# Kernel optimization log

Hardware: AMD Instinct MI355X
Metric: run time of the kernel (lower is better)

The kernel has to match this reference:

```python
import jax, jax.numpy as jnp
import numpy as np

EMBED_DIM = 64
HIDDEN_DIM = 320
CONTEXT_DIM = 768

def setup_inputs() -> dict:
    key = jax.random.key(0)
    k1, k2, k3, k4, k5 = jax.random.split(key, 5)
    B, T, S = 4, 4096, 4096
    tokens = jax.random.normal(k1, (B, T, HIDDEN_DIM), dtype=jnp.float32)
    context = jax.random.normal(k2, (B, S, CONTEXT_DIM), dtype=jnp.float32)
    # nn.Linear(in, out, bias=False) weights, stored as [out, in] like torch
    sq = 1.0 / np.sqrt(HIDDEN_DIM)
    sk = 1.0 / np.sqrt(CONTEXT_DIM)
    Wq = jax.random.uniform(k3, (EMBED_DIM, HIDDEN_DIM), minval=-sq, maxval=sq, dtype=jnp.float32)
    Wk = jax.random.uniform(k4, (EMBED_DIM, CONTEXT_DIM), minval=-sk, maxval=sk, dtype=jnp.float32)
    Wv = jax.random.uniform(k5, (HIDDEN_DIM, CONTEXT_DIM), minval=-sk, maxval=sk, dtype=jnp.float32)
    return {"tokens": tokens, "context": context, "Wq": Wq, "Wk": Wk, "Wv": Wv}

def reference(tokens, context, Wq, Wk, Wv):
    # Q: [B,T,E], K: [B,S,E], V: [B,S,Hd]
    Q = jnp.einsum('bth,eh->bte', tokens, Wq)
    K = jnp.einsum('bsc,ec->bse', context, Wk)
    V = jnp.einsum('bsc,hc->bsh', context, Wv)
    scores = jnp.einsum('bte,bse->bts', Q, K) / np.sqrt(EMBED_DIM)
    attn = jax.nn.softmax(scores, axis=-1)  # [B,T,S] full score matrix as in original
    ctx_vecs = jnp.einsum('bts,bsh->bth', attn, V)
    return ctx_vecs
```

## Files before the change

kernel.cpp:

```cpp
#include <hip/hip_runtime.h>
#include <hip/hip_bf16.h>

typedef _Float16 half4_t  __attribute__((ext_vector_type(4)));
typedef _Float16 half8_t  __attribute__((ext_vector_type(8)));
typedef float    float4_t __attribute__((ext_vector_type(4)));

#define MFMA16x32(a, b, c) __builtin_amdgcn_mfma_f32_16x16x32_f16(a, b, c, 0, 0, 0)

static constexpr int Tn = 4096, Sn = 4096, Hn = 320;

__device__ __forceinline__ void async16(const _Float16* g, _Float16* l) {
  __builtin_amdgcn_global_load_lds(
      (const __attribute__((address_space(1))) void*)g,
      (__attribute__((address_space(3))) void*)l, 16, 0, 0);
}

template <int KTOT, int NT>
__global__ __launch_bounds__(256, 2)
void proj_kernel(const float* __restrict__ A, const float* __restrict__ W,
                 _Float16* __restrict__ out, float sc) {
  constexpr int NCH = KTOT / 64;
  constexpr int NTIL = NT / 16;
  __shared__ alignas(16) _Float16 Ach[64 * 72];
  __shared__ alignas(16) _Float16 Bch[NT * 72];

  const int tid = threadIdx.x, w = tid >> 6, lane = tid & 63;
  const int G = lane >> 4, l15 = lane & 15;
  const int m0 = blockIdx.x * 64, n0 = blockIdx.y * NT;

  float4_t acc[NTIL];
#pragma unroll
  for (int nt = 0; nt < NTIL; ++nt) acc[nt] = {0.f, 0.f, 0.f, 0.f};

  float4_t areg[4], wreg[NTIL];
  auto ldA = [&](int kc) {
#pragma unroll
    for (int t = 0; t < 4; ++t) {
      int idx = t * 256 + tid;
      areg[t] = *(const float4_t*)(A + (size_t)(m0 + (idx >> 4)) * KTOT + kc * 64 + (idx & 15) * 4);
    }
  };
  auto ldW = [&](int kc) {
#pragma unroll
    for (int t = 0; t < NTIL; ++t) {
      int idx = t * 256 + tid;
      wreg[t] = *(const float4_t*)(W + (size_t)(n0 + (idx >> 4)) * KTOT + kc * 64 + (idx & 15) * 4);
    }
  };

  ldA(0); ldW(0);
  for (int kc = 0; kc < NCH; ++kc) {
    __syncthreads();
#pragma unroll
    for (int t = 0; t < 4; ++t) {
      int idx = t * 256 + tid;
      half4_t h = {(_Float16)areg[t][0], (_Float16)areg[t][1], (_Float16)areg[t][2], (_Float16)areg[t][3]};
      *(half4_t*)(Ach + (idx >> 4) * 72 + (idx & 15) * 4) = h;
    }
#pragma unroll
    for (int t = 0; t < NTIL; ++t) {
      int idx = t * 256 + tid;
      half4_t h = {(_Float16)wreg[t][0], (_Float16)wreg[t][1], (_Float16)wreg[t][2], (_Float16)wreg[t][3]};
      *(half4_t*)(Bch + (idx >> 4) * 72 + (idx & 15) * 4) = h;
    }
    __syncthreads();
    if (kc + 1 < NCH) { ldA(kc + 1); ldW(kc + 1); }
#pragma unroll
    for (int c = 0; c < 2; ++c) {
      half8_t af = *(const half8_t*)(Ach + (w * 16 + l15) * 72 + c * 32 + 8 * G);
#pragma unroll
      for (int nt = 0; nt < NTIL; ++nt) {
        half8_t bf = *(const half8_t*)(Bch + (nt * 16 + l15) * 72 + c * 32 + 8 * G);
        acc[nt] = MFMA16x32(af, bf, acc[nt]);
      }
    }
  }

  if constexpr (NT == 64) {
#pragma unroll
    for (int nt = 0; nt < NTIL; ++nt)
#pragma unroll
      for (int r = 0; r < 4; ++r)
        out[(size_t)(m0 + w * 16 + 4 * G + r) * 64 + nt * 16 + l15] = (_Float16)(acc[nt][r] * sc);
  } else {
    __syncthreads();
#pragma unroll
    for (int nt = 0; nt < NTIL; ++nt) {
      half4_t h = {(_Float16)acc[nt][0], (_Float16)acc[nt][1], (_Float16)acc[nt][2], (_Float16)acc[nt][3]};
      *(half4_t*)(Bch + (nt * 16 + l15) * 72 + w * 16 + 4 * G) = h;
    }
    __syncthreads();
#pragma unroll
    for (int rep = 0; rep < 5; ++rep) {
      int idx = w * 5 + rep;
      int c2 = idx / 10, htl = idx % 10;
      half8_t fr = *(const half8_t*)(Bch + (htl * 16 + l15) * 72 + c2 * 32 + 8 * G);
      int sg = m0 + c2 * 32;
      int b = sg >> 12, c2b = (sg & 4095) >> 5;
      int htg = blockIdx.y * 10 + htl;
      *(half8_t*)(out + ((size_t)((b * 128 + c2b) * 20 + htg)) * 512 + lane * 8) = fr;
    }
  }
}

__global__ __launch_bounds__(256, 2)
void flash_kernel(const _Float16* __restrict__ Qg, const _Float16* __restrict__ Kg,
                  const _Float16* __restrict__ Vt, _Float16* __restrict__ Op,
                  float* __restrict__ lp) {
  __shared__ alignas(16) _Float16 kbuf[32 * 72];
  __shared__ alignas(16) _Float16 pbuf[64 * 72];
  __shared__ alignas(16) _Float16 vbuf[2][10240];
  __shared__ float lred[4][32];

  const int tid = threadIdx.x, w = tid >> 6, lane = tid & 63;
  const int G = lane >> 4, l15 = lane & 15;
  const int bx = blockIdx.x;
  const int b = (bx & 7) >> 1, sh = bx & 1, tb = bx >> 3;
  const int tblk = tb * 64, sbase = sh * 2048;
  const int th = w >> 1, stile = w & 1;
  const int kr = tid >> 3, kc8 = (tid & 7) * 8;

  half8_t qf[2][2];
#pragma unroll
  for (int tt = 0; tt < 2; ++tt)
#pragma unroll
    for (int c = 0; c < 2; ++c)
      qf[tt][c] = *(const half8_t*)(Qg + (size_t)(b * Tn + tblk + th * 32 + tt * 16 + l15) * 64 + c * 32 + 8 * G);

  float4_t oacc[2][5][2];
  float4_t oa[4][5];
#pragma unroll
  for (int tt = 0; tt < 4; ++tt)
#pragma unroll
    for (int ht = 0; ht < 5; ++ht) oa[tt][ht] = {0.f, 0.f, 0.f, 0.f};
  float la[2] = {0.f, 0.f};

  const size_t vbase = (size_t)b * 1310720;

  {
    uint4 k0 = *(const uint4*)(Kg + (size_t)(b * Sn + sbase + kr) * 64 + kc8);
    *(uint4*)(&kbuf[kr * 72 + kc8]) = k0;
    const size_t voff = vbase + (size_t)(sh * 64) * 10240;
#pragma unroll
    for (int r = 0; r < 5; ++r) {
      int off = (w * 5 + r) * 512 + lane * 8;
      async16(Vt + voff + off, &vbuf[0][off]);
    }
  }
  __syncthreads();

  for (int n = 0; n < 64; ++n) {
    const int cb = n & 1;
    const bool more = (n < 63);
    uint4 kst;
    if (more)
      kst = *(const uint4*)(Kg + (size_t)(b * Sn + sbase + (n + 1) * 32 + kr) * 64 + kc8);

    float4_t sa[2] = {{0.f, 0.f, 0.f, 0.f}, {0.f, 0.f, 0.f, 0.f}};
#pragma unroll
    for (int c = 0; c < 2; ++c) {
      half8_t af = *(const half8_t*)(&kbuf[(stile * 16 + l15) * 72 + c * 32 + 8 * G]);
#pragma unroll
      for (int tt = 0; tt < 2; ++tt) sa[tt] = MFMA16x32(af, qf[tt][c], sa[tt]);
    }
#pragma unroll
    for (int tt = 0; tt < 2; ++tt) {
      float e0 = exp2f(sa[tt][0]), e1 = exp2f(sa[tt][1]);
      float e2 = exp2f(sa[tt][2]), e3 = exp2f(sa[tt][3]);
      la[tt] += (e0 + e1) + (e2 + e3);
      half4_t p = {(_Float16)e0, (_Float16)e1, (_Float16)e2, (_Float16)e3};
      *(half4_t*)(&pbuf[(th * 32 + tt * 16 + l15) * 72 + stile * 16 + 4 * G]) = p;
    }
    __syncthreads();

    if (more) {
      const size_t voff = vbase + (size_t)(sh * 64 + n + 1) * 10240;
#pragma unroll
      for (int r = 0; r < 5; ++r) {
        int off = (w * 5 + r) * 512 + lane * 8;
        async16(Vt + voff + off, &vbuf[1 - cb][off]);
      }
      *(uint4*)(&kbuf[kr * 72 + kc8]) = kst;
    }

    half8_t pa[4];
#pragma unroll
    for (int tt = 0; tt < 4; ++tt)
      pa[tt] = *(const half8_t*)(&pbuf[(tt * 16 + l15) * 72 + 8 * G]);
#pragma unroll
    for (int ht = 0; ht < 5; ++ht) {
      half8_t vb = *(const half8_t*)(&vbuf[cb][(w * 5 + ht) * 512 + lane * 8]);
#pragma unroll
      for (int tt = 0; tt < 4; ++tt) oa[tt][ht] = MFMA16x32(pa[tt], vb, oa[tt][ht]);
    }
    __syncthreads();
  }

#pragma unroll
  for (int tt = 0; tt < 2; ++tt) {
    float v = la[tt];
    v += __shfl_xor(v, 16);
    v += __shfl_xor(v, 32);
    if (lane < 16) lred[w][tt * 16 + lane] = v;
  }
  __syncthreads();
  if (stile == 0 && lane < 16) {
#pragma unroll
    for (int tt = 0; tt < 2; ++tt) {
      float lt = lred[w][tt * 16 + lane] + lred[w + 1][tt * 16 + lane];
      lp[(size_t)sh * 16384 + b * Tn + tblk + th * 32 + tt * 16 + lane] = lt;
    }
  }
  _Float16* myO = Op + (size_t)sh * 5242880;
#pragma unroll
  for (int tt = 0; tt < 4; ++tt)
#pragma unroll
    for (int ht = 0; ht < 5; ++ht)
#pragma unroll
      for (int r = 0; r < 4; ++r)
        myO[(size_t)(b * Tn + tblk + tt * 16 + 4 * G + r) * Hn + w * 80 + ht * 16 + l15] =
            (_Float16)oa[tt][ht][r];
}

__global__ __launch_bounds__(256)
void combine_kernel(const _Float16* __restrict__ O0, const _Float16* __restrict__ O1,
                    const float* __restrict__ l0, const float* __restrict__ l1,
                    float* __restrict__ out) {
  const int tid = threadIdx.x;
  const int base = blockIdx.x * 1280;
#pragma unroll
  for (int it = 0; it < 5; ++it) {
    int lin = base + it * 256 + tid;
    int row = lin / 80;
    float inv = 1.0f / (l0[row] + l1[row]);
    half4_t a = *(const half4_t*)(O0 + (size_t)lin * 4);
    half4_t c = *(const half4_t*)(O1 + (size_t)lin * 4);
    float4_t o = {((float)a[0] + (float)c[0]) * inv, ((float)a[1] + (float)c[1]) * inv,
                  ((float)a[2] + (float)c[2]) * inv, ((float)a[3] + (float)c[3]) * inv};
    *(float4_t*)(out + (size_t)lin * 4) = o;
  }
}

extern "C" void kernel_launch(void* const* d_in, const int* in_sizes, int n_in,
                              void* d_out, int out_size, void* d_ws, size_t ws_size,
                              hipStream_t stream) {
  const float* tokens  = (const float*)d_in[0];
  const float* context = (const float*)d_in[1];
  const float* Wq      = (const float*)d_in[2];
  const float* Wk      = (const float*)d_in[3];
  const float* Wv      = (const float*)d_in[4];

  _Float16* Qws = (_Float16*)d_ws;
  _Float16* Kws = Qws + (size_t)1048576;
  _Float16* Vws = Kws + (size_t)1048576;
  _Float16* O0  = Vws + (size_t)5242880;
  _Float16* O1  = O0 + (size_t)5242880;
  float*    l0  = (float*)(O1 + (size_t)5242880);
  float*    l1  = l0 + 16384;

  const float qsc = 0.125f * 1.44269504088896f;
  proj_kernel<320, 64><<<dim3(256, 1), 256, 0, stream>>>(tokens, Wq, Qws, qsc);
  proj_kernel<768, 64><<<dim3(256, 1), 256, 0, stream>>>(context, Wk, Kws, 1.0f);
  proj_kernel<768, 160><<<dim3(256, 2), 256, 0, stream>>>(context, Wv, Vws, 1.0f);
  flash_kernel<<<dim3(512), 256, 0, stream>>>(Qws, Kws, Vws, O0, l0);
  combine_kernel<<<dim3(1024), 256, 0, stream>>>(O0, O1, l0, l1, (float*)d_out);
}
```

Measured before the change: 229.6 us.

## Fuse QKV projections, warp-specialize flash kernel, drop split-S combine

The three projection launches become one kernel that dispatches on block index. The flash kernel now uses 512-thread blocks where four warps compute QK^T and exp while four warps do PV with register-prefetched V, ping-ponged through double-buffered LDS. Each block walks the full S range, so the split-S partial outputs and the separate combine kernel go away, and normalization happens in the epilogue with fp32 output. This cuts launches and intermediate traffic but halves the grid to 256 blocks and doubles the serial loop length per block.

```diff
diff --git a/kernel.cpp b/kernel.cpp
--- a/kernel.cpp
+++ b/kernel.cpp
@@ -7,26 +7,16 @@
 
 #define MFMA16x32(a, b, c) __builtin_amdgcn_mfma_f32_16x16x32_f16(a, b, c, 0, 0, 0)
 
-static constexpr int Tn = 4096, Sn = 4096, Hn = 320;
-
-__device__ __forceinline__ void async16(const _Float16* g, _Float16* l) {
-  __builtin_amdgcn_global_load_lds(
-      (const __attribute__((address_space(1))) void*)g,
-      (__attribute__((address_space(3))) void*)l, 16, 0, 0);
-}
-
-template <int KTOT, int NT>
-__global__ __launch_bounds__(256, 2)
-void proj_kernel(const float* __restrict__ A, const float* __restrict__ W,
-                 _Float16* __restrict__ out, float sc) {
+template <int KTOT, int NT, int MODE>
+__device__ __forceinline__ void proj_body(const float* __restrict__ A,
+                                          const float* __restrict__ W,
+                                          _Float16* __restrict__ out, float sc,
+                                          int m0, int n0, int htg0,
+                                          _Float16* Ach, _Float16* Bch) {
   constexpr int NCH = KTOT / 64;
   constexpr int NTIL = NT / 16;
-  __shared__ alignas(16) _Float16 Ach[64 * 72];
-  __shared__ alignas(16) _Float16 Bch[NT * 72];
-
   const int tid = threadIdx.x, w = tid >> 6, lane = tid & 63;
   const int G = lane >> 4, l15 = lane & 15;
-  const int m0 = blockIdx.x * 64, n0 = blockIdx.y * NT;
 
   float4_t acc[NTIL];
 #pragma unroll
@@ -76,7 +66,7 @@
     }
   }
 
-  if constexpr (NT == 64) {
+  if constexpr (MODE <= 1) {
 #pragma unroll
     for (int nt = 0; nt < NTIL; ++nt)
 #pragma unroll
@@ -97,147 +87,167 @@
       half8_t fr = *(const half8_t*)(Bch + (htl * 16 + l15) * 72 + c2 * 32 + 8 * G);
       int sg = m0 + c2 * 32;
       int b = sg >> 12, c2b = (sg & 4095) >> 5;
-      int htg = blockIdx.y * 10 + htl;
+      int htg = htg0 + htl;
       *(half8_t*)(out + ((size_t)((b * 128 + c2b) * 20 + htg)) * 512 + lane * 8) = fr;
     }
   }
 }
 
 __global__ __launch_bounds__(256, 2)
+void qkv_proj_kernel(const float* __restrict__ tokens, const float* __restrict__ context,
+                     const float* __restrict__ Wq, const float* __restrict__ Wk,
+                     const float* __restrict__ Wv, _Float16* __restrict__ Q,
+                     _Float16* __restrict__ K, _Float16* __restrict__ V) {
+  __shared__ alignas(16) _Float16 smem[16128];
+  _Float16* Ach = smem;
+  _Float16* Bch = smem + 64 * 72;
+  const int bx = blockIdx.x;
+  const float qsc = 0.125f * 1.44269504088896f;
+  if (bx < 512) {
+    int y = bx >> 8, mb = bx & 255;
+    proj_body<768, 160, 2>(context, Wv, V, 1.0f, mb * 64, y * 160, y * 10, Ach, Bch);
+  } else if (bx < 768) {
+    proj_body<768, 64, 1>(context, Wk, K, 1.0f, (bx - 512) * 64, 0, 0, Ach, Bch);
+  } else {
+    proj_body<320, 64, 0>(tokens, Wq, Q, qsc, (bx - 768) * 64, 0, 0, Ach, Bch);
+  }
+}
+
+__global__ __launch_bounds__(512, 2)
 void flash_kernel(const _Float16* __restrict__ Qg, const _Float16* __restrict__ Kg,
-                  const _Float16* __restrict__ Vt, _Float16* __restrict__ Op,
-                  float* __restrict__ lp) {
-  __shared__ alignas(16) _Float16 kbuf[32 * 72];
-  __shared__ alignas(16) _Float16 pbuf[64 * 72];
-  __shared__ alignas(16) _Float16 vbuf[2][10240];
-  __shared__ float lred[4][32];
+                  const _Float16* __restrict__ Vt, float* __restrict__ out) {
+  __shared__ alignas(16) _Float16 kbuf[2][2048];
+  __shared__ alignas(16) _Float16 pbuf[2][2048];
+  __shared__ float larr[2][4][16];
+  __shared__ float linv[64];
 
   const int tid = threadIdx.x, w = tid >> 6, lane = tid & 63;
   const int G = lane >> 4, l15 = lane & 15;
   const int bx = blockIdx.x;
-  const int b = (bx & 7) >> 1, sh = bx & 1, tb = bx >> 3;
-  const int tblk = tb * 64, sbase = sh * 2048;
-  const int th = w >> 1, stile = w & 1;
-  const int kr = tid >> 3, kc8 = (tid & 7) * 8;
+  const int b = (bx & 7) >> 1;
+  const int tblk = ((bx & 1) * 32 + (bx >> 3)) * 64;
+
+  const bool is_pv = (w < 4);
+  const int sw = w - 4;
+  const int stile = sw & 1, tthalf = sw >> 1;
+  const int t2 = tid & 255;
+  const int s_loc = t2 >> 3, e8 = t2 & 7;
+  const int kdst = ((s_loc >> 4) * 2 + (e8 >> 2)) * 512 + ((e8 & 3) * 16 + (s_loc & 15)) * 8;
+  const _Float16* kg = Kg + (size_t)(b * 4096) * 64 + s_loc * 64 + e8 * 8;
+  const _Float16* vt_b = Vt + (size_t)b * 1310720;
 
   half8_t qf[2][2];
-#pragma unroll
-  for (int tt = 0; tt < 2; ++tt)
+  float la[2] = {0.f, 0.f};
+  float4_t oa[4][5];
+#pragma unroll
+  for (int tt = 0; tt < 4; ++tt)
+#pragma unroll
+    for (int ht = 0; ht < 5; ++ht) oa[tt][ht] = {0.f, 0.f, 0.f, 0.f};
+  half8_t vcur[5], vnxt[5];
+
+  if (!is_pv) {
+    uint4 k0 = *(const uint4*)(kg);
+    uint4 k1 = *(const uint4*)(kg + 2048);
+    *(uint4*)(&kbuf[0][kdst]) = k0;
+    *(uint4*)(&kbuf[1][kdst]) = k1;
+#pragma unroll
+    for (int tt2 = 0; tt2 < 2; ++tt2) {
+      int tt = tthalf * 2 + tt2;
+#pragma unroll
+      for (int c = 0; c < 2; ++c)
+        qf[tt2][c] = *(const half8_t*)(Qg + (size_t)(b * 4096 + tblk + tt * 16 + l15) * 64 + c * 32 + 8 * G);
+    }
+  }
+  __syncthreads();
+
+  if (is_pv) {
+#pragma unroll
+    for (int ht = 0; ht < 5; ++ht)
+      vcur[ht] = *(const half8_t*)(vt_b + (w * 5 + ht) * 512 + lane * 8);
+  } else {
+    half8_t af[2];
 #pragma unroll
     for (int c = 0; c < 2; ++c)
-      qf[tt][c] = *(const half8_t*)(Qg + (size_t)(b * Tn + tblk + th * 32 + tt * 16 + l15) * 64 + c * 32 + 8 * G);
-
-  float4_t oacc[2][5][2];
-  float4_t oa[4][5];
-#pragma unroll
-  for (int tt = 0; tt < 4; ++tt)
-#pragma unroll
-    for (int ht = 0; ht < 5; ++ht) oa[tt][ht] = {0.f, 0.f, 0.f, 0.f};
-  float la[2] = {0.f, 0.f};
-
-  const size_t vbase = (size_t)b * 1310720;
-
-  {
-    uint4 k0 = *(const uint4*)(Kg + (size_t)(b * Sn + sbase + kr) * 64 + kc8);
-    *(uint4*)(&kbuf[kr * 72 + kc8]) = k0;
-    const size_t voff = vbase + (size_t)(sh * 64) * 10240;
-#pragma unroll
-    for (int r = 0; r < 5; ++r) {
-      int off = (w * 5 + r) * 512 + lane * 8;
-      async16(Vt + voff + off, &vbuf[0][off]);
-    }
-  }
-  __syncthreads();
-
-  for (int n = 0; n < 64; ++n) {
-    const int cb = n & 1;
-    const bool more = (n < 63);
-    uint4 kst;
-    if (more)
-      kst = *(const uint4*)(Kg + (size_t)(b * Sn + sbase + (n + 1) * 32 + kr) * 64 + kc8);
-
-    float4_t sa[2] = {{0.f, 0.f, 0.f, 0.f}, {0.f, 0.f, 0.f, 0.f}};
-#pragma unroll
-    for (int c = 0; c < 2; ++c) {
-      half8_t af = *(const half8_t*)(&kbuf[(stile * 16 + l15) * 72 + c * 32 + 8 * G]);
-#pragma unroll
-      for (int tt = 0; tt < 2; ++tt) sa[tt] = MFMA16x32(af, qf[tt][c], sa[tt]);
-    }
-#pragma unroll
-    for (int tt = 0; tt < 2; ++tt) {
-      float e0 = exp2f(sa[tt][0]), e1 = exp2f(sa[tt][1]);
-      float e2 = exp2f(sa[tt][2]), e3 = exp2f(sa[tt][3]);
-      la[tt] += (e0 + e1) + (e2 + e3);
+      af[c] = *(const half8_t*)(&kbuf[0][(stile * 2 + c) * 512 + lane * 8]);
+#pragma unroll
+    for (int tt2 = 0; tt2 < 2; ++tt2) {
+      float4_t sa = {0.f, 0.f, 0.f, 0.f};
+#pragma unroll
+      for (int c = 0; c < 2; ++c) sa = MFMA16x32(af[c], qf[tt2][c], sa);
+      float e0 = exp2f(sa[0]), e1 = exp2f(sa[1]), e2 = exp2f(sa[2]), e3 = exp2f(sa[3]);
+      la[tt2] += (e0 + e1) + (e2 + e3);
+      int tt = tthalf * 2 + tt2;
+      int Gp = stile * 2 + (G >> 1);
       half4_t p = {(_Float16)e0, (_Float16)e1, (_Float16)e2, (_Float16)e3};
-      *(half4_t*)(&pbuf[(th * 32 + tt * 16 + l15) * 72 + stile * 16 + 4 * G]) = p;
-    }
-    __syncthreads();
-
-    if (more) {
-      const size_t voff = vbase + (size_t)(sh * 64 + n + 1) * 10240;
-#pragma unroll
-      for (int r = 0; r < 5; ++r) {
-        int off = (w * 5 + r) * 512 + lane * 8;
-        async16(Vt + voff + off, &vbuf[1 - cb][off]);
-      }
-      *(uint4*)(&kbuf[kr * 72 + kc8]) = kst;
-    }
-
-    half8_t pa[4];
+      *(half4_t*)(&pbuf[0][tt * 512 + (Gp * 16 + l15) * 8 + 4 * (G & 1)]) = p;
+    }
+  }
+  __syncthreads();
+
+  for (int i = 0; i < 128; ++i) {
+    if (is_pv) {
+      if (i < 127) {
+#pragma unroll
+        for (int ht = 0; ht < 5; ++ht)
+          vnxt[ht] = *(const half8_t*)(vt_b + (size_t)(i + 1) * 10240 + (w * 5 + ht) * 512 + lane * 8);
+      }
+      half8_t pa[4];
+#pragma unroll
+      for (int tt = 0; tt < 4; ++tt)
+        pa[tt] = *(const half8_t*)(&pbuf[i & 1][tt * 512 + lane * 8]);
+#pragma unroll
+      for (int ht = 0; ht < 5; ++ht)
+#pragma unroll
+        for (int tt = 0; tt < 4; ++tt) oa[tt][ht] = MFMA16x32(pa[tt], vcur[ht], oa[tt][ht]);
+#pragma unroll
+      for (int ht = 0; ht < 5; ++ht) vcur[ht] = vnxt[ht];
+    } else if (i < 127) {
+      uint4 kreg;
+      if (i < 126) kreg = *(const uint4*)(kg + (size_t)(i + 2) * 2048);
+      half8_t af[2];
+#pragma unroll
+      for (int c = 0; c < 2; ++c)
+        af[c] = *(const half8_t*)(&kbuf[(i + 1) & 1][(stile * 2 + c) * 512 + lane * 8]);
+#pragma unroll
+      for (int tt2 = 0; tt2 < 2; ++tt2) {
+        float4_t sa = {0.f, 0.f, 0.f, 0.f};
+#pragma unroll
+        for (int c = 0; c < 2; ++c) sa = MFMA16x32(af[c], qf[tt2][c], sa);
+        float e0 = exp2f(sa[0]), e1 = exp2f(sa[1]), e2 = exp2f(sa[2]), e3 = exp2f(sa[3]);
+        la[tt2] += (e0 + e1) + (e2 + e3);
+        int tt = tthalf * 2 + tt2;
+        int Gp = stile * 2 + (G >> 1);
+        half4_t p = {(_Float16)e0, (_Float16)e1, (_Float16)e2, (_Float16)e3};
+        *(half4_t*)(&pbuf[(i + 1) & 1][tt * 512 + (Gp * 16 + l15) * 8 + 4 * (G & 1)]) = p;
+      }
+      if (i < 126) *(uint4*)(&kbuf[i & 1][kdst]) = kreg;
+    }
+    __syncthreads();
+  }
+
+  if (!is_pv) {
+#pragma unroll
+    for (int tt2 = 0; tt2 < 2; ++tt2) {
+      float v = la[tt2];
+      v += __shfl_xor(v, 16);
+      v += __shfl_xor(v, 32);
+      if (lane < 16) larr[stile][tthalf * 2 + tt2][l15] = v;
+    }
+  }
+  __syncthreads();
+  if (tid < 64) linv[tid] = 1.0f / (larr[0][tid >> 4][tid & 15] + larr[1][tid >> 4][tid & 15]);
+  __syncthreads();
+  if (is_pv) {
 #pragma unroll
     for (int tt = 0; tt < 4; ++tt)
-      pa[tt] = *(const half8_t*)(&pbuf[(tt * 16 + l15) * 72 + 8 * G]);
-#pragma unroll
-    for (int ht = 0; ht < 5; ++ht) {
-      half8_t vb = *(const half8_t*)(&vbuf[cb][(w * 5 + ht) * 512 + lane * 8]);
-#pragma unroll
-      for (int tt = 0; tt < 4; ++tt) oa[tt][ht] = MFMA16x32(pa[tt], vb, oa[tt][ht]);
-    }
-    __syncthreads();
-  }
-
-#pragma unroll
-  for (int tt = 0; tt < 2; ++tt) {
-    float v = la[tt];
-    v += __shfl_xor(v, 16);
-    v += __shfl_xor(v, 32);
-    if (lane < 16) lred[w][tt * 16 + lane] = v;
-  }
-  __syncthreads();
-  if (stile == 0 && lane < 16) {
-#pragma unroll
-    for (int tt = 0; tt < 2; ++tt) {
-      float lt = lred[w][tt * 16 + lane] + lred[w + 1][tt * 16 + lane];
-      lp[(size_t)sh * 16384 + b * Tn + tblk + th * 32 + tt * 16 + lane] = lt;
-    }
-  }
-  _Float16* myO = Op + (size_t)sh * 5242880;
-#pragma unroll
-  for (int tt = 0; tt < 4; ++tt)
-#pragma unroll
-    for (int ht = 0; ht < 5; ++ht)
-#pragma unroll
-      for (int r = 0; r < 4; ++r)
-        myO[(size_t)(b * Tn + tblk + tt * 16 + 4 * G + r) * Hn + w * 80 + ht * 16 + l15] =
-            (_Float16)oa[tt][ht][r];
-}
-
-__global__ __launch_bounds__(256)
-void combine_kernel(const _Float16* __restrict__ O0, const _Float16* __restrict__ O1,
-                    const float* __restrict__ l0, const float* __restrict__ l1,
-                    float* __restrict__ out) {
-  const int tid = threadIdx.x;
-  const int base = blockIdx.x * 1280;
-#pragma unroll
-  for (int it = 0; it < 5; ++it) {
-    int lin = base + it * 256 + tid;
-    int row = lin / 80;
-    float inv = 1.0f / (l0[row] + l1[row]);
-    half4_t a = *(const half4_t*)(O0 + (size_t)lin * 4);
-    half4_t c = *(const half4_t*)(O1 + (size_t)lin * 4);
-    float4_t o = {((float)a[0] + (float)c[0]) * inv, ((float)a[1] + (float)c[1]) * inv,
-                  ((float)a[2] + (float)c[2]) * inv, ((float)a[3] + (float)c[3]) * inv};
-    *(float4_t*)(out + (size_t)lin * 4) = o;
+#pragma unroll
+      for (int r = 0; r < 4; ++r) {
+        float inv = linv[tt * 16 + 4 * G + r];
+        size_t row = (size_t)(b * 4096 + tblk + tt * 16 + 4 * G + r) * 320;
+#pragma unroll
+        for (int ht = 0; ht < 5; ++ht)
+          out[row + w * 80 + ht * 16 + l15] = oa[tt][ht][r] * inv;
+      }
   }
 }
 
@@ -253,15 +263,8 @@
   _Float16* Qws = (_Float16*)d_ws;
   _Float16* Kws = Qws + (size_t)1048576;
   _Float16* Vws = Kws + (size_t)1048576;
-  _Float16* O0  = Vws + (size_t)5242880;
-  _Float16* O1  = O0 + (size_t)5242880;
-  float*    l0  = (float*)(O1 + (size_t)5242880);
-  float*    l1  = l0 + 16384;
-
-  const float qsc = 0.125f * 1.44269504088896f;
-  proj_kernel<320, 64><<<dim3(256, 1), 256, 0, stream>>>(tokens, Wq, Qws, qsc);
-  proj_kernel<768, 64><<<dim3(256, 1), 256, 0, stream>>>(context, Wk, Kws, 1.0f);
-  proj_kernel<768, 160><<<dim3(256, 2), 256, 0, stream>>>(context, Wv, Vws, 1.0f);
-  flash_kernel<<<dim3(512), 256, 0, stream>>>(Qws, Kws, Vws, O0, l0);
-  combine_kernel<<<dim3(1024), 256, 0, stream>>>(O0, O1, l0, l1, (float*)d_out);
-}
+
+  qkv_proj_kernel<<<dim3(1024), 256, 0, stream>>>(tokens, context, Wq, Wk, Wv,
+                                                  Qws, Kws, Vws);
+  flash_kernel<<<dim3(256), 512, 0, stream>>>(Qws, Kws, Vws, (float*)d_out);
+}
```

Result: faster. 205.0 us (-10.7%).

## Fuse Q/K/V projections into one kernel and deepen flash pipeline with register V

Applied to the files above, without the earlier changes.

Adds a small kernel that casts the weights to fp16 once. The three projection launches are merged into one 512-thread kernel in which K and V share a single pass over the context rows, so context is read once instead of twice. The flash kernel now loads V straight into registers from the pre-tiled layout instead of async LDS copies, keeps a 4-deep K/P ring buffer in LDS with swizzled P indexing, and has one barrier per step instead of two. The price is higher register pressure and more complex prefetch logic, with clamped prefetch indices that issue some redundant loads at the tail.

```diff
diff --git a/kernel.cpp b/kernel.cpp
--- a/kernel.cpp
+++ b/kernel.cpp
@@ -7,99 +7,176 @@
 
 #define MFMA16x32(a, b, c) __builtin_amdgcn_mfma_f32_16x16x32_f16(a, b, c, 0, 0, 0)
 
-static constexpr int Tn = 4096, Sn = 4096, Hn = 320;
-
-__device__ __forceinline__ void async16(const _Float16* g, _Float16* l) {
-  __builtin_amdgcn_global_load_lds(
-      (const __attribute__((address_space(1))) void*)g,
-      (__attribute__((address_space(3))) void*)l, 16, 0, 0);
-}
-
-template <int KTOT, int NT>
-__global__ __launch_bounds__(256, 2)
-void proj_kernel(const float* __restrict__ A, const float* __restrict__ W,
-                 _Float16* __restrict__ out, float sc) {
-  constexpr int NCH = KTOT / 64;
-  constexpr int NTIL = NT / 16;
-  __shared__ alignas(16) _Float16 Ach[64 * 72];
-  __shared__ alignas(16) _Float16 Bch[NT * 72];
-
-  const int tid = threadIdx.x, w = tid >> 6, lane = tid & 63;
+__global__ __launch_bounds__(256)
+void wcast_kernel(const float* __restrict__ Wq, const float* __restrict__ Wk,
+                  const float* __restrict__ Wv, _Float16* __restrict__ Wqh,
+                  _Float16* __restrict__ Wkh, _Float16* __restrict__ Wvh) {
+  const int bx = blockIdx.x, tid = threadIdx.x;
+  const float* src; _Float16* dst; int idx;
+  if (bx < 20)       { src = Wq; dst = Wqh; idx = bx * 256 + tid; }
+  else if (bx < 68)  { src = Wk; dst = Wkh; idx = (bx - 20) * 256 + tid; }
+  else               { src = Wv; dst = Wvh; idx = (bx - 68) * 256 + tid; }
+  float4_t v = *(const float4_t*)(src + (size_t)idx * 4);
+  half4_t h = {(_Float16)v[0], (_Float16)v[1], (_Float16)v[2], (_Float16)v[3]};
+  *(half4_t*)(dst + (size_t)idx * 4) = h;
+}
+
+__global__ __launch_bounds__(512, 2)
+void proj_kernel(const float* __restrict__ tokens, const float* __restrict__ context,
+                 const _Float16* __restrict__ Wqh, const _Float16* __restrict__ Wkh,
+                 const _Float16* __restrict__ Wvh, _Float16* __restrict__ Qws,
+                 _Float16* __restrict__ Kws, _Float16* __restrict__ Vws) {
+  __shared__ alignas(16) _Float16 smem[20480];
+  _Float16* Ach = smem;
+  _Float16* Wch = smem + 5120;
+
+  const int bx = blockIdx.x, tid = threadIdx.x;
+  const int w = tid >> 6, lane = tid & 63;
   const int G = lane >> 4, l15 = lane & 15;
-  const int m0 = blockIdx.x * 64, n0 = blockIdx.y * NT;
-
-  float4_t acc[NTIL];
-#pragma unroll
-  for (int nt = 0; nt < NTIL; ++nt) acc[nt] = {0.f, 0.f, 0.f, 0.f};
-
-  float4_t areg[4], wreg[NTIL];
-  auto ldA = [&](int kc) {
-#pragma unroll
-    for (int t = 0; t < 4; ++t) {
-      int idx = t * 256 + tid;
-      areg[t] = *(const float4_t*)(A + (size_t)(m0 + (idx >> 4)) * KTOT + kc * 64 + (idx & 15) * 4);
-    }
-  };
-  auto ldW = [&](int kc) {
-#pragma unroll
-    for (int t = 0; t < NTIL; ++t) {
-      int idx = t * 256 + tid;
-      wreg[t] = *(const float4_t*)(W + (size_t)(n0 + (idx >> 4)) * KTOT + kc * 64 + (idx & 15) * 4);
-    }
-  };
-
-  ldA(0); ldW(0);
-  for (int kc = 0; kc < NCH; ++kc) {
+
+  if (bx < 128) {
+    const int m0 = bx * 128;
+    const int mg = w >> 2, ng = w & 3;
+
+    float4_t acc[4][6];
+#pragma unroll
+    for (int mi = 0; mi < 4; ++mi)
+#pragma unroll
+      for (int nt = 0; nt < 6; ++nt) acc[mi][nt] = {0.f, 0.f, 0.f, 0.f};
+
+    float4_t areg[2];
+    half8_t wreg[3];
+    auto ldA = [&](int kc) {
+#pragma unroll
+      for (int t = 0; t < 2; ++t) {
+        int slot = t * 512 + tid, row = slot >> 3, c4 = slot & 7;
+        areg[t] = *(const float4_t*)(context + (size_t)(m0 + row) * 768 + kc * 32 + c4 * 4);
+      }
+    };
+    auto ldW = [&](int kc) {
+#pragma unroll
+      for (int t = 0; t < 3; ++t) {
+        int slot = t * 512 + tid, row = slot >> 2, c8 = slot & 3;
+        const _Float16* p = (row < 64) ? (Wkh + (size_t)row * 768)
+                                       : (Wvh + (size_t)(row - 64) * 768);
+        wreg[t] = *(const half8_t*)(p + kc * 32 + c8 * 8);
+      }
+    };
+
+    ldA(0); ldW(0);
+    for (int kc = 0; kc < 24; ++kc) {
+      __syncthreads();
+#pragma unroll
+      for (int t = 0; t < 2; ++t) {
+        int slot = t * 512 + tid, row = slot >> 3, c4 = slot & 7;
+        half4_t h = {(_Float16)areg[t][0], (_Float16)areg[t][1],
+                     (_Float16)areg[t][2], (_Float16)areg[t][3]};
+        *(half4_t*)(Ach + row * 40 + c4 * 4) = h;
+      }
+#pragma unroll
+      for (int t = 0; t < 3; ++t) {
+        int slot = t * 512 + tid, row = slot >> 2, c8 = slot & 3;
+        *(half8_t*)(Wch + row * 40 + c8 * 8) = wreg[t];
+      }
+      __syncthreads();
+      if (kc + 1 < 24) { ldA(kc + 1); ldW(kc + 1); }
+      half8_t af[4], bf[6];
+#pragma unroll
+      for (int mi = 0; mi < 4; ++mi)
+        af[mi] = *(const half8_t*)(Ach + (mg * 64 + mi * 16 + l15) * 40 + 8 * G);
+#pragma unroll
+      for (int nt = 0; nt < 6; ++nt)
+        bf[nt] = *(const half8_t*)(Wch + ((ng * 6 + nt) * 16 + l15) * 40 + 8 * G);
+#pragma unroll
+      for (int mi = 0; mi < 4; ++mi)
+#pragma unroll
+        for (int nt = 0; nt < 6; ++nt) acc[mi][nt] = MFMA16x32(af[mi], bf[nt], acc[mi][nt]);
+    }
+
+    if (ng == 0) {
+#pragma unroll
+      for (int mi = 0; mi < 4; ++mi)
+#pragma unroll
+        for (int nt = 0; nt < 4; ++nt)
+#pragma unroll
+          for (int r = 0; r < 4; ++r)
+            Kws[(size_t)(m0 + mg * 64 + mi * 16 + 4 * G + r) * 64 + nt * 16 + l15] =
+                (_Float16)acc[mi][nt][r];
+    }
     __syncthreads();
-#pragma unroll
-    for (int t = 0; t < 4; ++t) {
-      int idx = t * 256 + tid;
-      half4_t h = {(_Float16)areg[t][0], (_Float16)areg[t][1], (_Float16)areg[t][2], (_Float16)areg[t][3]};
-      *(half4_t*)(Ach + (idx >> 4) * 72 + (idx & 15) * 4) = h;
-    }
-#pragma unroll
-    for (int t = 0; t < NTIL; ++t) {
-      int idx = t * 256 + tid;
-      half4_t h = {(_Float16)wreg[t][0], (_Float16)wreg[t][1], (_Float16)wreg[t][2], (_Float16)wreg[t][3]};
-      *(half4_t*)(Bch + (idx >> 4) * 72 + (idx & 15) * 4) = h;
-    }
-    __syncthreads();
-    if (kc + 1 < NCH) { ldA(kc + 1); ldW(kc + 1); }
-#pragma unroll
-    for (int c = 0; c < 2; ++c) {
-      half8_t af = *(const half8_t*)(Ach + (w * 16 + l15) * 72 + c * 32 + 8 * G);
-#pragma unroll
-      for (int nt = 0; nt < NTIL; ++nt) {
-        half8_t bf = *(const half8_t*)(Bch + (nt * 16 + l15) * 72 + c * 32 + 8 * G);
+    _Float16* scr = smem + w * 1152;
+    const int b = bx >> 5;
+#pragma unroll
+    for (int nt = 0; nt < 6; ++nt) {
+      int jt = ng * 6 + nt;
+      if (jt < 4) continue;
+      int htg = jt - 4;
+#pragma unroll
+      for (int mi = 0; mi < 4; ++mi) {
+        half4_t h = {(_Float16)acc[mi][nt][0], (_Float16)acc[mi][nt][1],
+                     (_Float16)acc[mi][nt][2], (_Float16)acc[mi][nt][3]};
+        *(half4_t*)(scr + l15 * 72 + mi * 16 + 4 * G) = h;
+      }
+#pragma unroll
+      for (int c2 = 0; c2 < 2; ++c2) {
+        half8_t fr = *(const half8_t*)(scr + l15 * 72 + c2 * 32 + 8 * G);
+        int c2b = (bx & 31) * 4 + mg * 2 + c2;
+        *(half8_t*)(Vws + ((size_t)((b * 128 + c2b) * 20 + htg)) * 512 + lane * 8) = fr;
+      }
+    }
+  } else {
+    const int m0 = (bx - 128) * 128;
+    const float qsc = 0.125f * 1.44269504088896f;
+
+    float4_t acc[4];
+#pragma unroll
+    for (int nt = 0; nt < 4; ++nt) acc[nt] = {0.f, 0.f, 0.f, 0.f};
+
+    float4_t areg[2];
+    half8_t wreg;
+    auto ldA = [&](int kc) {
+#pragma unroll
+      for (int t = 0; t < 2; ++t) {
+        int slot = t * 512 + tid, row = slot >> 3, c4 = slot & 7;
+        areg[t] = *(const float4_t*)(tokens + (size_t)(m0 + row) * 320 + kc * 32 + c4 * 4);
+      }
+    };
+    auto ldW = [&](int kc) {
+      if (tid < 256) {
+        int row = tid >> 2, c8 = tid & 3;
+        wreg = *(const half8_t*)(Wqh + (size_t)row * 320 + kc * 32 + c8 * 8);
+      }
+    };
+
+    ldA(0); ldW(0);
+    for (int kc = 0; kc < 10; ++kc) {
+      __syncthreads();
+#pragma unroll
+      for (int t = 0; t < 2; ++t) {
+        int slot = t * 512 + tid, row = slot >> 3, c4 = slot & 7;
+        half4_t h = {(_Float16)areg[t][0], (_Float16)areg[t][1],
+                     (_Float16)areg[t][2], (_Float16)areg[t][3]};
+        *(half4_t*)(Ach + row * 40 + c4 * 4) = h;
+      }
+      if (tid < 256) {
+        int row = tid >> 2, c8 = tid & 3;
+        *(half8_t*)(Wch + row * 40 + c8 * 8) = wreg;
+      }
+      __syncthreads();
+      if (kc + 1 < 10) { ldA(kc + 1); ldW(kc + 1); }
+      half8_t af = *(const half8_t*)(Ach + (w * 16 + l15) * 40 + 8 * G);
+#pragma unroll
+      for (int nt = 0; nt < 4; ++nt) {
+        half8_t bf = *(const half8_t*)(Wch + (nt * 16 + l15) * 40 + 8 * G);
         acc[nt] = MFMA16x32(af, bf, acc[nt]);
       }
     }
-  }
-
-  if constexpr (NT == 64) {
-#pragma unroll
-    for (int nt = 0; nt < NTIL; ++nt)
+#pragma unroll
+    for (int nt = 0; nt < 4; ++nt)
 #pragma unroll
       for (int r = 0; r < 4; ++r)
-        out[(size_t)(m0 + w * 16 + 4 * G + r) * 64 + nt * 16 + l15] = (_Float16)(acc[nt][r] * sc);
-  } else {
-    __syncthreads();
-#pragma unroll
-    for (int nt = 0; nt < NTIL; ++nt) {
-      half4_t h = {(_Float16)acc[nt][0], (_Float16)acc[nt][1], (_Float16)acc[nt][2], (_Float16)acc[nt][3]};
-      *(half4_t*)(Bch + (nt * 16 + l15) * 72 + w * 16 + 4 * G) = h;
-    }
-    __syncthreads();
-#pragma unroll
-    for (int rep = 0; rep < 5; ++rep) {
-      int idx = w * 5 + rep;
-      int c2 = idx / 10, htl = idx % 10;
-      half8_t fr = *(const half8_t*)(Bch + (htl * 16 + l15) * 72 + c2 * 32 + 8 * G);
-      int sg = m0 + c2 * 32;
-      int b = sg >> 12, c2b = (sg & 4095) >> 5;
-      int htg = blockIdx.y * 10 + htl;
-      *(half8_t*)(out + ((size_t)((b * 128 + c2b) * 20 + htg)) * 512 + lane * 8) = fr;
-    }
+        Qws[(size_t)(m0 + w * 16 + 4 * G + r) * 64 + nt * 16 + l15] =
+            (_Float16)(acc[nt][r] * qsc);
   }
 }
 
@@ -107,27 +184,34 @@
 void flash_kernel(const _Float16* __restrict__ Qg, const _Float16* __restrict__ Kg,
                   const _Float16* __restrict__ Vt, _Float16* __restrict__ Op,
                   float* __restrict__ lp) {
-  __shared__ alignas(16) _Float16 kbuf[32 * 72];
-  __shared__ alignas(16) _Float16 pbuf[64 * 72];
-  __shared__ alignas(16) _Float16 vbuf[2][10240];
-  __shared__ float lred[4][32];
+  __shared__ alignas(16) _Float16 kbuf[4 * 2048];
+  __shared__ alignas(16) _Float16 pbuf[4 * 2048];
+  __shared__ float larr[2][4][16];
 
   const int tid = threadIdx.x, w = tid >> 6, lane = tid & 63;
   const int G = lane >> 4, l15 = lane & 15;
   const int bx = blockIdx.x;
-  const int b = (bx & 7) >> 1, sh = bx & 1, tb = bx >> 3;
-  const int tblk = tb * 64, sbase = sh * 2048;
-  const int th = w >> 1, stile = w & 1;
-  const int kr = tid >> 3, kc8 = (tid & 7) * 8;
+  const int xcd = bx & 7, b = xcd >> 1, sh = xcd & 1;
+  const int tblk = (bx >> 3) * 64;
+  const int st = w & 1, th = w >> 1;
+
+  const int sB = tid >> 6, sL = tid & 63;
+  const int s_loc = (sB >> 1) * 16 + (sL & 15);
+  const int e0 = (sB & 1) * 32 + (sL >> 4) * 8;
+  const _Float16* kg = Kg + (size_t)(b * 4096 + sh * 2048 + s_loc) * 64 + e0;
+
+  const int pidx = (lane ^ ((lane >> 3) & 3)) * 8;
+  int idxp = (st * 2 + (G >> 1)) * 16 + l15;
+  idxp ^= (idxp >> 3) & 3;
+  const int pw = idxp * 8 + 4 * (G & 1);
 
   half8_t qf[2][2];
 #pragma unroll
-  for (int tt = 0; tt < 2; ++tt)
+  for (int tt2 = 0; tt2 < 2; ++tt2)
 #pragma unroll
     for (int c = 0; c < 2; ++c)
-      qf[tt][c] = *(const half8_t*)(Qg + (size_t)(b * Tn + tblk + th * 32 + tt * 16 + l15) * 64 + c * 32 + 8 * G);
-
-  float4_t oacc[2][5][2];
+      qf[tt2][c] = *(const half8_t*)(Qg + (size_t)(b * 4096 + tblk + (th * 2 + tt2) * 16 + l15) * 64 + c * 32 + 8 * G);
+
   float4_t oa[4][5];
 #pragma unroll
   for (int tt = 0; tt < 4; ++tt)
@@ -135,82 +219,84 @@
     for (int ht = 0; ht < 5; ++ht) oa[tt][ht] = {0.f, 0.f, 0.f, 0.f};
   float la[2] = {0.f, 0.f};
 
-  const size_t vbase = (size_t)b * 1310720;
-
-  {
-    uint4 k0 = *(const uint4*)(Kg + (size_t)(b * Sn + sbase + kr) * 64 + kc8);
-    *(uint4*)(&kbuf[kr * 72 + kc8]) = k0;
-    const size_t voff = vbase + (size_t)(sh * 64) * 10240;
-#pragma unroll
-    for (int r = 0; r < 5; ++r) {
-      int off = (w * 5 + r) * 512 + lane * 8;
-      async16(Vt + voff + off, &vbuf[0][off]);
-    }
+  const size_t vbase = (size_t)(b * 128 + sh * 64) * 20;
+
+  auto kload = [&](int c) { return *(const uint4*)(kg + (size_t)c * 2048); };
+  auto kwrite = [&](int buf, uint4 v) { *(uint4*)(&kbuf[buf * 2048 + tid * 8]) = v; };
+  auto vload = [&](int c, half8_t v[5]) {
+#pragma unroll
+    for (int ht = 0; ht < 5; ++ht)
+      v[ht] = *(const half8_t*)(Vt + (vbase + (size_t)c * 20 + w * 5 + ht) * 512 + lane * 8);
+  };
+  auto st_step = [&](int buf) {
+    half8_t af0 = *(const half8_t*)(&kbuf[buf * 2048 + (st * 2) * 512 + lane * 8]);
+    half8_t af1 = *(const half8_t*)(&kbuf[buf * 2048 + (st * 2 + 1) * 512 + lane * 8]);
+#pragma unroll
+    for (int tt2 = 0; tt2 < 2; ++tt2) {
+      float4_t sa = {0.f, 0.f, 0.f, 0.f};
+      sa = MFMA16x32(af0, qf[tt2][0], sa);
+      sa = MFMA16x32(af1, qf[tt2][1], sa);
+      float ex0 = exp2f(sa[0]), ex1 = exp2f(sa[1]), ex2 = exp2f(sa[2]), ex3 = exp2f(sa[3]);
+      la[tt2] += (ex0 + ex1) + (ex2 + ex3);
+      half4_t p = {(_Float16)ex0, (_Float16)ex1, (_Float16)ex2, (_Float16)ex3};
+      *(half4_t*)(&pbuf[buf * 2048 + (th * 2 + tt2) * 512 + pw]) = p;
+    }
+  };
+  auto pv_step = [&](int buf, const half8_t vv[5]) {
+    half8_t pa[4];
+#pragma unroll
+    for (int tt = 0; tt < 4; ++tt)
+      pa[tt] = *(const half8_t*)(&pbuf[buf * 2048 + tt * 512 + pidx]);
+#pragma unroll
+    for (int ht = 0; ht < 5; ++ht)
+#pragma unroll
+      for (int tt = 0; tt < 4; ++tt) oa[tt][ht] = MFMA16x32(pa[tt], vv[ht], oa[tt][ht]);
+  };
+
+  half8_t vA[5], vB[5], vnA[5], vnB[5];
+  uint4 ka, kb;
+
+  ka = kload(0); kb = kload(1);
+  kwrite(0, ka); kwrite(1, kb);
+  ka = kload(2); kb = kload(3);
+  __syncthreads();
+  st_step(0);
+  st_step(1);
+  vload(0, vA); vload(1, vB);
+  kwrite(2, ka); kwrite(3, kb);
+  ka = kload(4); kb = kload(5);
+  __syncthreads();
+
+#pragma unroll 2
+  for (int j = 0; j < 32; ++j) {
+    const int c0 = 2 * j, c1 = c0 + 1;
+    const int vc0 = (c0 + 2 > 63) ? 63 : c0 + 2;
+    const int vc1 = (c1 + 2 > 63) ? 63 : c1 + 2;
+    vload(vc0, vnA); vload(vc1, vnB);
+    const int kc0 = (c0 + 6 > 63) ? 63 : c0 + 6;
+    const int kc1 = (c1 + 6 > 63) ? 63 : c1 + 6;
+    uint4 nka = kload(kc0), nkb = kload(kc1);
+    if (j < 31) { st_step((c0 + 2) & 3); st_step((c1 + 2) & 3); }
+    pv_step(c0 & 3, vA);
+    pv_step(c1 & 3, vB);
+    kwrite((c0 + 4) & 3, ka); kwrite((c1 + 4) & 3, kb);
+    ka = nka; kb = nkb;
+#pragma unroll
+    for (int ht = 0; ht < 5; ++ht) { vA[ht] = vnA[ht]; vB[ht] = vnB[ht]; }
+    __syncthreads();
+  }
+
+#pragma unroll
+  for (int tt2 = 0; tt2 < 2; ++tt2) {
+    float v = la[tt2];
+    v += __shfl_xor(v, 16);
+    v += __shfl_xor(v, 32);
+    if (lane < 16) larr[st][th * 2 + tt2][lane] = v;
   }
   __syncthreads();
-
-  for (int n = 0; n < 64; ++n) {
-    const int cb = n & 1;
-    const bool more = (n < 63);
-    uint4 kst;
-    if (more)
-      kst = *(const uint4*)(Kg + (size_t)(b * Sn + sbase + (n + 1) * 32 + kr) * 64 + kc8);
-
-    float4_t sa[2] = {{0.f, 0.f, 0.f, 0.f}, {0.f, 0.f, 0.f, 0.f}};
-#pragma unroll
-    for (int c = 0; c < 2; ++c) {
-      half8_t af = *(const half8_t*)(&kbuf[(stile * 16 + l15) * 72 + c * 32 + 8 * G]);
-#pragma unroll
-      for (int tt = 0; tt < 2; ++tt) sa[tt] = MFMA16x32(af, qf[tt][c], sa[tt]);
-    }
-#pragma unroll
-    for (int tt = 0; tt < 2; ++tt) {
-      float e0 = exp2f(sa[tt][0]), e1 = exp2f(sa[tt][1]);
-      float e2 = exp2f(sa[tt][2]), e3 = exp2f(sa[tt][3]);
-      la[tt] += (e0 + e1) + (e2 + e3);
-      half4_t p = {(_Float16)e0, (_Float16)e1, (_Float16)e2, (_Float16)e3};
-      *(half4_t*)(&pbuf[(th * 32 + tt * 16 + l15) * 72 + stile * 16 + 4 * G]) = p;
-    }
-    __syncthreads();
-
-    if (more) {
-      const size_t voff = vbase + (size_t)(sh * 64 + n + 1) * 10240;
-#pragma unroll
-      for (int r = 0; r < 5; ++r) {
-        int off = (w * 5 + r) * 512 + lane * 8;
-        async16(Vt + voff + off, &vbuf[1 - cb][off]);
-      }
-      *(uint4*)(&kbuf[kr * 72 + kc8]) = kst;
-    }
-
-    half8_t pa[4];
-#pragma unroll
-    for (int tt = 0; tt < 4; ++tt)
-      pa[tt] = *(const half8_t*)(&pbuf[(tt * 16 + l15) * 72 + 8 * G]);
-#pragma unroll
-    for (int ht = 0; ht < 5; ++ht) {
-      half8_t vb = *(const half8_t*)(&vbuf[cb][(w * 5 + ht) * 512 + lane * 8]);
-#pragma unroll
-      for (int tt = 0; tt < 4; ++tt) oa[tt][ht] = MFMA16x32(pa[tt], vb, oa[tt][ht]);
-    }
-    __syncthreads();
-  }
-
-#pragma unroll
-  for (int tt = 0; tt < 2; ++tt) {
-    float v = la[tt];
-    v += __shfl_xor(v, 16);
-    v += __shfl_xor(v, 32);
-    if (lane < 16) lred[w][tt * 16 + lane] = v;
-  }
-  __syncthreads();
-  if (stile == 0 && lane < 16) {
-#pragma unroll
-    for (int tt = 0; tt < 2; ++tt) {
-      float lt = lred[w][tt * 16 + lane] + lred[w + 1][tt * 16 + lane];
-      lp[(size_t)sh * 16384 + b * Tn + tblk + th * 32 + tt * 16 + lane] = lt;
-    }
-  }
+  if (tid < 64)
+    lp[(size_t)sh * 16384 + b * 4096 + tblk + tid] =
+        larr[0][tid >> 4][tid & 15] + larr[1][tid >> 4][tid & 15];
   _Float16* myO = Op + (size_t)sh * 5242880;
 #pragma unroll
   for (int tt = 0; tt < 4; ++tt)
@@ -218,7 +304,7 @@
     for (int ht = 0; ht < 5; ++ht)
 #pragma unroll
       for (int r = 0; r < 4; ++r)
-        myO[(size_t)(b * Tn + tblk + tt * 16 + 4 * G + r) * Hn + w * 80 + ht * 16 + l15] =
+        myO[(size_t)(b * 4096 + tblk + tt * 16 + 4 * G + r) * 320 + (w * 5 + ht) * 16 + l15] =
             (_Float16)oa[tt][ht][r];
 }
 
@@ -254,14 +340,16 @@
   _Float16* Kws = Qws + (size_t)1048576;
   _Float16* Vws = Kws + (size_t)1048576;
   _Float16* O0  = Vws + (size_t)5242880;
-  _Float16* O1  = O0 + (size_t)5242880;
+  _Float16* O1  = O0  + (size_t)5242880;
   float*    l0  = (float*)(O1 + (size_t)5242880);
   float*    l1  = l0 + 16384;
-
-  const float qsc = 0.125f * 1.44269504088896f;
-  proj_kernel<320, 64><<<dim3(256, 1), 256, 0, stream>>>(tokens, Wq, Qws, qsc);
-  proj_kernel<768, 64><<<dim3(256, 1), 256, 0, stream>>>(context, Wk, Kws, 1.0f);
-  proj_kernel<768, 160><<<dim3(256, 2), 256, 0, stream>>>(context, Wv, Vws, 1.0f);
+  _Float16* Wqh = (_Float16*)(l1 + 16384);
+  _Float16* Wkh = Wqh + 20480;
+  _Float16* Wvh = Wkh + 49152;
+
+  wcast_kernel<<<dim3(308), 256, 0, stream>>>(Wq, Wk, Wv, Wqh, Wkh, Wvh);
+  proj_kernel<<<dim3(256), 512, 0, stream>>>(tokens, context, Wqh, Wkh, Wvh,
+                                             Qws, Kws, Vws);
   flash_kernel<<<dim3(512), 256, 0, stream>>>(Qws, Kws, Vws, O0, l0);
   combine_kernel<<<dim3(1024), 256, 0, stream>>>(O0, O1, l0, l1, (float*)d_out);
 }
```

Result: faster. 210.8 us (-8.2%).
